# Kernel tuning notes

Hardware: AMD Instinct MI355X
Metric: run time of the kernel (lower is better)

## Reference

```python
import jax, jax.numpy as jnp
import numpy as np

N = 400000   # nodes; must equal E because the original code computes `out + x` with out per-edge
E = 400000   # edges
HID = 128
HEADS = 4
NEG_SLOPE = 0.01  # torch F.leaky_relu default


def setup_inputs() -> dict:
    key = jax.random.key(0)
    k1, k2, k3, k4 = jax.random.split(key, 4)
    x = jax.random.normal(k1, (N, HID), dtype=jnp.float32)
    edge_index = jax.random.randint(k2, (2, E), 0, N, dtype=jnp.int64)
    # xavier-uniform-ish scale for the attention parameter [1, heads, 2*hidden]
    lim_a = float(np.sqrt(6.0 / (1 + HEADS * 2 * HID)))
    attention = jax.random.uniform(k3, (1, HEADS, 2 * HID), jnp.float32, -lim_a, lim_a)
    lim_w = float(np.sqrt(1.0 / (HID * HEADS)))
    W = jax.random.uniform(k4, (HID, HID * HEADS), jnp.float32, -lim_w, lim_w)
    b = jnp.zeros((HID,), jnp.float32)
    return {"x": x, "edge_index": edge_index, "attention": attention, "W": W, "b": b}


def _scatter_softmax(s, seg, num_segments):
    # softmax over edges grouped by destination node index `seg` (axis 0)
    m = jax.lax.stop_gradient(jax.ops.segment_max(s, seg, num_segments=num_segments))
    ex = jnp.exp(s - m[seg])
    denom = jax.ops.segment_sum(ex, seg, num_segments=num_segments)
    return ex / denom[seg]


def reference(x, edge_index, attention, W, b):
    row, col = edge_index[0], edge_index[1]
    # [E, 2*HID] per-edge concatenated features
    ef = jnp.concatenate([x[row], x[col]], axis=-1)
    # per-head scores: (ef[:,None,:] * attention).sum(-1) -> [E, HEADS]
    scores = jnp.einsum('ef,hf->eh', ef, attention[0])
    scores = jax.nn.leaky_relu(scores, NEG_SLOPE)
    scores = jax.nn.softmax(scores, axis=1)      # softmax across heads (as in source)
    # dropout(p=0.1) -> identity in eval mode
    alpha = _scatter_softmax(scores, row, N)     # [E, HEADS] per-destination softmax
    # per-head weighted source features, concatenated over heads -> [E, HEADS*HID]
    feats = (alpha[:, :, None] * x[col][:, None, :]).reshape(E, HEADS * HID)
    out = feats @ W.T + b                        # Linear(hidden*heads -> hidden)
    return out + x
```

## Files before the change

kernel.cpp:

```cpp
#include <hip/hip_runtime.h>

#define NN 400000
#define NE 400000

typedef __attribute__((ext_vector_type(4))) float f32x4;
typedef __attribute__((ext_vector_type(8))) short s16x8;
typedef unsigned short ushort_t;

__device__ __forceinline__ ushort_t f2bf(float f) {
    union { float f; unsigned int u; } c;
    c.f = f;
    unsigned int u = c.u;
    u = u + 0x7fffu + ((u >> 16) & 1u);
    return (ushort_t)(u >> 16);
}
__device__ __forceinline__ float bf2f(ushort_t v) {
    union { unsigned int u; float f; } c;
    c.u = ((unsigned int)v) << 16;
    return c.f;
}

__global__ void k_detect(const int* __restrict__ ei_raw, int* __restrict__ flag) {
    if (threadIdx.x == 0 && blockIdx.x == 0) {
        int is64 = 1;
        for (int i = 0; i < 64; i++)
            if (ei_raw[2 * i + 1] != 0) { is64 = 0; break; }
        flag[0] = is64;
    }
}

__global__ void k_cvt_idx(const int* __restrict__ ei_raw, const int* __restrict__ flag,
                          int* __restrict__ ei32) {
    const int i = blockIdx.x * 256 + threadIdx.x;
    const int f = flag[0];
    ei32[i] = f ? ei_raw[2 * i] : ei_raw[i];
}

__global__ void k_wcvt(const float* __restrict__ W, ushort_t* __restrict__ wsw) {
    const int t = blockIdx.x * 256 + threadIdx.x;
    const int c = t >> 13;
    const int h = c >> 1, half = c & 1;
    const int si = t & 8191;
    const int i = si >> 6;
    const int inner = (si * 2) & 127;
    const int koff = inner ^ ((i & 7) << 4);
    const int j = half * 64 + (koff >> 1);
    wsw[t] = f2bf(W[i * 512 + h * 128 + j]);
}

__global__ void k_uv_cvt(const float* __restrict__ x, const float* __restrict__ att,
                         ushort_t* __restrict__ xbf, float* __restrict__ uv) {
    const int lane = threadIdx.x & 63;
    const int wid = threadIdx.x >> 6;
    const int g = lane & 15;
    const int ns = lane >> 4;

    float areg[8][8];
#pragma unroll
    for (int h = 0; h < 4; h++) {
        const f32x4 fa = *(const f32x4*)(att + h * 256 + g * 8);
        const f32x4 fb = *(const f32x4*)(att + h * 256 + g * 8 + 4);
        const f32x4 ba = *(const f32x4*)(att + h * 256 + 128 + g * 8);
        const f32x4 bb = *(const f32x4*)(att + h * 256 + 128 + g * 8 + 4);
#pragma unroll
        for (int m = 0; m < 4; m++) {
            areg[h][m] = fa[m];     areg[h][4 + m] = fb[m];
            areg[4 + h][m] = ba[m]; areg[4 + h][4 + m] = bb[m];
        }
    }

    for (int tile = blockIdx.x; tile < NN / 32; tile += gridDim.x) {
        const int nb = tile * 32 + wid * 8 + ns;
#pragma unroll
        for (int t = 0; t < 2; t++) {
            const int n = nb + t * 4;
            const f32x4 xa = *(const f32x4*)(x + (size_t)n * 128 + g * 8);
            const f32x4 xb = *(const f32x4*)(x + (size_t)n * 128 + g * 8 + 4);
            s16x8 pk;
#pragma unroll
            for (int m = 0; m < 4; m++) { pk[m] = (short)f2bf(xa[m]); pk[4 + m] = (short)f2bf(xb[m]); }
            *(s16x8*)(xbf + (size_t)n * 128 + g * 8) = pk;
            float r[8];
#pragma unroll
            for (int v = 0; v < 8; v++) {
                float s = 0.f;
#pragma unroll
                for (int m = 0; m < 4; m++) s += xa[m] * areg[v][m];
#pragma unroll
                for (int m = 0; m < 4; m++) s += xb[m] * areg[v][4 + m];
                r[v] = s;
            }
#pragma unroll
            for (int mask = 1; mask <= 4; mask <<= 1)
#pragma unroll
                for (int v = 0; v < 8; v++) r[v] += __shfl_xor(r[v], mask, 64);
            const int gv = g & 7;
            float s = r[0];
#pragma unroll
            for (int v = 1; v < 8; v++) s = (gv == v) ? r[v] : s;
            s += __shfl_xor(s, 8, 64);
            if (g < 8) uv[(size_t)n * 8 + g] = s;
        }
    }
}

__global__ void k_edge(const int* __restrict__ ei, const float* __restrict__ uv,
                       float* __restrict__ p, float* __restrict__ denom) {
    const int e = blockIdx.x * 256 + threadIdx.x;
    if (e >= NE) return;
    const int row = ei[e];
    const int col = ei[NE + e];
    const f32x4 u = *(const f32x4*)(uv + (size_t)row * 8);
    const f32x4 v = *(const f32x4*)(uv + (size_t)col * 8 + 4);
    float s[4];
    float mx = -1e30f;
#pragma unroll
    for (int h = 0; h < 4; h++) {
        float t = u[h] + v[h];
        t = t > 0.f ? t : 0.01f * t;
        s[h] = t;
        mx = fmaxf(mx, t);
    }
    float ex[4], sum = 0.f;
#pragma unroll
    for (int h = 0; h < 4; h++) { ex[h] = __expf(s[h] - mx); sum += ex[h]; }
    const float inv = 1.f / sum;
    f32x4 pv;
#pragma unroll
    for (int h = 0; h < 4; h++) pv[h] = __expf(ex[h] * inv);
    *(f32x4*)(p + (size_t)e * 4) = pv;
#pragma unroll
    for (int h = 0; h < 4; h++) atomicAdd(denom + (size_t)row * 4 + h, pv[h]);
}

__global__ void k_alpha(const int* __restrict__ ei, const float* __restrict__ p,
                        const float* __restrict__ denom, float* __restrict__ alpha_t) {
    const int e = blockIdx.x * 256 + threadIdx.x;
    if (e >= NE) return;
    const int row = ei[e];
    const f32x4 pv = *(const f32x4*)(p + (size_t)e * 4);
    const f32x4 dv = *(const f32x4*)(denom + (size_t)row * 4);
#pragma unroll
    for (int h = 0; h < 4; h++) alpha_t[(size_t)h * NE + e] = pv[h] / dv[h];
}

__global__ __launch_bounds__(512) void k_gemm(
    const ushort_t* __restrict__ xbf, const int* __restrict__ ei,
    const float* __restrict__ alpha_t, const ushort_t* __restrict__ wsw,
    const float* __restrict__ bias, float* __restrict__ out)
{
    __shared__ __align__(16) ushort_t Asm[128 * 128];
    __shared__ __align__(16) ushort_t Bsm[2][128 * 64];

    const int tid = threadIdx.x;
    const int lane = tid & 63;
    const int wid = tid >> 6;
    const int wr = wid >> 1;
    const int wc = wid & 1;
    const int e0 = blockIdx.x * 128;

#define B_ISSUE(c, buf) do {                                                         \
    const ushort_t* base_ = wsw + (c) * 8192;                                        \
    _Pragma("unroll")                                                                \
    for (int sub_ = 0; sub_ < 2; sub_++) {                                           \
        const int woff_ = wid * 2048 + sub_ * 1024;                                  \
        __builtin_amdgcn_global_load_lds(                                            \
            (const __attribute__((address_space(1))) unsigned int*)(base_ + woff_ / 2 + lane * 8), \
            (__attribute__((address_space(3))) unsigned int*)((char*)Bsm[buf] + woff_), \
            16, 0, 0);                                                               \
    } } while (0)

    {
        const int e_loc = tid >> 2, part = tid & 3;
        const int col = ei[NE + e0 + e_loc];
        const ushort_t* src = xbf + (size_t)col * 128 + part * 32;
#pragma unroll
        for (int q = 0; q < 4; q++) {
            const s16x8 v = *(const s16x8*)(src + q * 8);
            const int byte = (e_loc * 256 + part * 64 + q * 16) ^ ((e_loc & 7) << 4);
            *(s16x8*)((char*)Asm + byte) = v;
        }
    }
    B_ISSUE(0, 0);
    __syncthreads();

    s16x8 afr[4][2];
#pragma unroll
    for (int jq = 0; jq < 4; jq++)
#pragma unroll
        for (int eb = 0; eb < 2; eb++) {
            const int row = wr * 32 + eb * 16 + (lane & 15);
            const int byte = (row * 256 + jq * 64 + (lane >> 4) * 16) ^ ((row & 7) << 4);
            afr[jq][eb] = *(const s16x8*)((const char*)Asm + byte);
        }

    f32x4 fin[2][4];
#pragma unroll
    for (int eb = 0; eb < 2; eb++)
#pragma unroll
        for (int ib = 0; ib < 4; ib++) fin[eb][ib] = {0.f, 0.f, 0.f, 0.f};

#pragma unroll
    for (int h = 0; h < 4; h++) {
        f32x4 acc[2][4];
#pragma unroll
        for (int half = 0; half < 2; half++) {
            const int c = h * 2 + half;
            if (c < 7) B_ISSUE(c + 1, (c + 1) & 1);
#pragma unroll
            for (int ks = 0; ks < 2; ks++) {
                const int jq = half * 2 + ks;
#pragma unroll
                for (int ib = 0; ib < 4; ib++) {
                    const int row = wc * 64 + ib * 16 + (lane & 15);
                    const int byte = (row * 128 + ks * 64 + (lane >> 4) * 16) ^ ((row & 7) << 4);
                    const s16x8 bfr = *(const s16x8*)((const char*)Bsm[c & 1] + byte);
#pragma unroll
                    for (int eb = 0; eb < 2; eb++) {
                        if (jq == 0)
                            acc[eb][ib] = __builtin_amdgcn_mfma_f32_16x16x32_bf16(
                                afr[0][eb], bfr, (f32x4){0.f, 0.f, 0.f, 0.f}, 0, 0, 0);
                        else
                            acc[eb][ib] = __builtin_amdgcn_mfma_f32_16x16x32_bf16(
                                afr[jq][eb], bfr, acc[eb][ib], 0, 0, 0);
                    }
                }
            }
            __syncthreads();
        }
#pragma unroll
        for (int eb = 0; eb < 2; eb++) {
            const int ebase = wr * 32 + eb * 16 + (lane >> 4) * 4;
            const f32x4 av = *(const f32x4*)(alpha_t + (size_t)h * NE + e0 + ebase);
#pragma unroll
            for (int ib = 0; ib < 4; ib++)
#pragma unroll
                for (int r = 0; r < 4; r++) fin[eb][ib][r] += av[r] * acc[eb][ib][r];
        }
    }

#pragma unroll
    for (int ib = 0; ib < 4; ib++) {
        const int i = wc * 64 + ib * 16 + (lane & 15);
        const float bb = bias[i];
#pragma unroll
        for (int eb = 0; eb < 2; eb++) {
#pragma unroll
            for (int r = 0; r < 4; r++) {
                const int e = e0 + wr * 32 + eb * 16 + (lane >> 4) * 4 + r;
                const size_t off = (size_t)e * 128 + i;
                out[off] = fin[eb][ib][r] + bb + bf2f(xbf[off]);
            }
        }
    }
#undef B_ISSUE
}

extern "C" void kernel_launch(void* const* d_in, const int* in_sizes, int n_in,
                              void* d_out, int out_size, void* d_ws, size_t ws_size,
                              hipStream_t stream) {
    const float* x      = (const float*)d_in[0];
    const int*   ei_raw = (const int*)d_in[1];
    const float* att    = (const float*)d_in[2];
    const float* W      = (const float*)d_in[3];
    const float* b      = (const float*)d_in[4];
    float* out = (float*)d_out;

    char* ws = (char*)d_ws;
    float*    uv      = (float*)(ws);
    float*    p       = (float*)(ws + 12800000);
    float*    denom   = (float*)(ws + 19200000);
    float*    alpha_t = (float*)(ws + 25600000);
    ushort_t* wsw     = (ushort_t*)(ws + 32000000);
    int*      flag    = (int*)(ws + 32200000);
    int*      ei32    = (int*)(ws + 32200064);
    ushort_t* xbf     = (ushort_t*)(ws + 35400192);

    hipMemsetAsync(denom, 0, (size_t)NN * 4 * sizeof(float), stream);
    k_detect<<<1, 64, 0, stream>>>(ei_raw, flag);
    k_cvt_idx<<<2 * NE / 256, 256, 0, stream>>>(ei_raw, flag, ei32);
    k_wcvt<<<256, 256, 0, stream>>>(W, wsw);
    k_uv_cvt<<<2048, 256, 0, stream>>>(x, att, xbf, uv);
    k_edge<<<(NE + 255) / 256, 256, 0, stream>>>(ei32, uv, p, denom);
    k_alpha<<<(NE + 255) / 256, 256, 0, stream>>>(ei32, p, denom, alpha_t);
    k_gemm<<<NE / 128, 512, 0, stream>>>(xbf, ei32, alpha_t, wsw, b, out);
}
```

Measured before the change: 310.4 us.

## Hold W in registers and stream gathered x tiles in a persistent GEMM loop

The GEMM kernel is restructured so each wave keeps its slice of the bf16 weight matrix resident in registers for all four heads. Each block then loops over 25 tiles of 32 edges, gathering x rows from global memory straight into MFMA fragments with double buffering. This removes the per-block LDS staging of A and B and the repeated global_load_lds of W with its barriers. The costs are higher register pressure (launch bounds of 512 threads with 2 blocks), uncoalesced 16-byte gathers per lane, and fewer blocks (500) to cover the GPU.

```diff
diff --git a/kernel.cpp b/kernel.cpp
--- a/kernel.cpp
+++ b/kernel.cpp
@@ -36,16 +36,9 @@
     ei32[i] = f ? ei_raw[2 * i] : ei_raw[i];
 }
 
-__global__ void k_wcvt(const float* __restrict__ W, ushort_t* __restrict__ wsw) {
-    const int t = blockIdx.x * 256 + threadIdx.x;
-    const int c = t >> 13;
-    const int h = c >> 1, half = c & 1;
-    const int si = t & 8191;
-    const int i = si >> 6;
-    const int inner = (si * 2) & 127;
-    const int koff = inner ^ ((i & 7) << 4);
-    const int j = half * 64 + (koff >> 1);
-    wsw[t] = f2bf(W[i * 512 + h * 128 + j]);
+__global__ void k_wcvt(const float* __restrict__ W, ushort_t* __restrict__ wbf) {
+    const int i = blockIdx.x * 256 + threadIdx.x;
+    wbf[i] = f2bf(W[i]);
 }
 
 __global__ void k_uv_cvt(const float* __restrict__ x, const float* __restrict__ att,
@@ -144,116 +137,92 @@
     for (int h = 0; h < 4; h++) alpha_t[(size_t)h * NE + e] = pv[h] / dv[h];
 }
 
-__global__ __launch_bounds__(512) void k_gemm(
+__global__ __launch_bounds__(512, 2) void k_gemm(
     const ushort_t* __restrict__ xbf, const int* __restrict__ ei,
-    const float* __restrict__ alpha_t, const ushort_t* __restrict__ wsw,
+    const float* __restrict__ alpha_t, const ushort_t* __restrict__ wbf,
     const float* __restrict__ bias, float* __restrict__ out)
 {
-    __shared__ __align__(16) ushort_t Asm[128 * 128];
-    __shared__ __align__(16) ushort_t Bsm[2][128 * 64];
+    __shared__ int col_s[800];
+    __shared__ float alp_s[4][800];
 
     const int tid = threadIdx.x;
     const int lane = tid & 63;
     const int wid = tid >> 6;
-    const int wr = wid >> 1;
-    const int wc = wid & 1;
-    const int e0 = blockIdx.x * 128;
-
-#define B_ISSUE(c, buf) do {                                                         \
-    const ushort_t* base_ = wsw + (c) * 8192;                                        \
-    _Pragma("unroll")                                                                \
-    for (int sub_ = 0; sub_ < 2; sub_++) {                                           \
-        const int woff_ = wid * 2048 + sub_ * 1024;                                  \
-        __builtin_amdgcn_global_load_lds(                                            \
-            (const __attribute__((address_space(1))) unsigned int*)(base_ + woff_ / 2 + lane * 8), \
-            (__attribute__((address_space(3))) unsigned int*)((char*)Bsm[buf] + woff_), \
-            16, 0, 0);                                                               \
-    } } while (0)
-
+    const int e0 = blockIdx.x * 800;
+
+    for (int j = tid; j < 800; j += 512) col_s[j] = ei[NE + e0 + j];
+#pragma unroll
+    for (int h = 0; h < 4; h++)
+        for (int j = tid; j < 800; j += 512) alp_s[h][j] = alpha_t[(size_t)h * NE + e0 + j];
+
+    s16x8 bfr[4][4];
     {
-        const int e_loc = tid >> 2, part = tid & 3;
-        const int col = ei[NE + e0 + e_loc];
-        const ushort_t* src = xbf + (size_t)col * 128 + part * 32;
-#pragma unroll
-        for (int q = 0; q < 4; q++) {
-            const s16x8 v = *(const s16x8*)(src + q * 8);
-            const int byte = (e_loc * 256 + part * 64 + q * 16) ^ ((e_loc & 7) << 4);
-            *(s16x8*)((char*)Asm + byte) = v;
-        }
-    }
-    B_ISSUE(0, 0);
+        const ushort_t* bbase = wbf + (wid * 16 + (lane & 15)) * 512 + (lane >> 4) * 8;
+#pragma unroll
+        for (int h = 0; h < 4; h++)
+#pragma unroll
+            for (int ks = 0; ks < 4; ks++)
+                bfr[h][ks] = *(const s16x8*)(bbase + h * 128 + ks * 32);
+    }
+    const float bias_r = bias[wid * 16 + (lane & 15)];
     __syncthreads();
 
-    s16x8 afr[4][2];
-#pragma unroll
-    for (int jq = 0; jq < 4; jq++)
+    const f32x4 zero = {0.f, 0.f, 0.f, 0.f};
+    s16x8 afA[2][4], afB[2][4];
+
+    auto LOADA = [&](int t, s16x8 (&af)[2][4]) {
 #pragma unroll
         for (int eb = 0; eb < 2; eb++) {
-            const int row = wr * 32 + eb * 16 + (lane & 15);
-            const int byte = (row * 256 + jq * 64 + (lane >> 4) * 16) ^ ((row & 7) << 4);
-            afr[jq][eb] = *(const s16x8*)((const char*)Asm + byte);
-        }
-
-    f32x4 fin[2][4];
-#pragma unroll
-    for (int eb = 0; eb < 2; eb++)
-#pragma unroll
-        for (int ib = 0; ib < 4; ib++) fin[eb][ib] = {0.f, 0.f, 0.f, 0.f};
-
-#pragma unroll
-    for (int h = 0; h < 4; h++) {
-        f32x4 acc[2][4];
-#pragma unroll
-        for (int half = 0; half < 2; half++) {
-            const int c = h * 2 + half;
-            if (c < 7) B_ISSUE(c + 1, (c + 1) & 1);
-#pragma unroll
-            for (int ks = 0; ks < 2; ks++) {
-                const int jq = half * 2 + ks;
-#pragma unroll
-                for (int ib = 0; ib < 4; ib++) {
-                    const int row = wc * 64 + ib * 16 + (lane & 15);
-                    const int byte = (row * 128 + ks * 64 + (lane >> 4) * 16) ^ ((row & 7) << 4);
-                    const s16x8 bfr = *(const s16x8*)((const char*)Bsm[c & 1] + byte);
-#pragma unroll
-                    for (int eb = 0; eb < 2; eb++) {
-                        if (jq == 0)
-                            acc[eb][ib] = __builtin_amdgcn_mfma_f32_16x16x32_bf16(
-                                afr[0][eb], bfr, (f32x4){0.f, 0.f, 0.f, 0.f}, 0, 0, 0);
-                        else
-                            acc[eb][ib] = __builtin_amdgcn_mfma_f32_16x16x32_bf16(
-                                afr[jq][eb], bfr, acc[eb][ib], 0, 0, 0);
-                    }
-                }
-            }
-            __syncthreads();
-        }
-#pragma unroll
-        for (int eb = 0; eb < 2; eb++) {
-            const int ebase = wr * 32 + eb * 16 + (lane >> 4) * 4;
-            const f32x4 av = *(const f32x4*)(alpha_t + (size_t)h * NE + e0 + ebase);
-#pragma unroll
-            for (int ib = 0; ib < 4; ib++)
-#pragma unroll
-                for (int r = 0; r < 4; r++) fin[eb][ib][r] += av[r] * acc[eb][ib][r];
-        }
-    }
-
-#pragma unroll
-    for (int ib = 0; ib < 4; ib++) {
-        const int i = wc * 64 + ib * 16 + (lane & 15);
-        const float bb = bias[i];
-#pragma unroll
-        for (int eb = 0; eb < 2; eb++) {
-#pragma unroll
-            for (int r = 0; r < 4; r++) {
-                const int e = e0 + wr * 32 + eb * 16 + (lane >> 4) * 4 + r;
+            const int c = col_s[t * 32 + eb * 16 + (lane & 15)];
+            const ushort_t* base = xbf + (size_t)c * 128 + (lane >> 4) * 8;
+#pragma unroll
+            for (int jq = 0; jq < 4; jq++)
+                af[eb][jq] = *(const s16x8*)(base + jq * 32);
+        }
+    };
+
+    auto TILE = [&](int t, s16x8 (&af)[2][4]) {
+        f32x4 fin0 = zero, fin1 = zero;
+#pragma unroll
+        for (int h = 0; h < 4; h++) {
+            f32x4 a0 = __builtin_amdgcn_mfma_f32_16x16x32_bf16(af[0][0], bfr[h][0], zero, 0, 0, 0);
+            f32x4 a1 = __builtin_amdgcn_mfma_f32_16x16x32_bf16(af[1][0], bfr[h][0], zero, 0, 0, 0);
+#pragma unroll
+            for (int ks = 1; ks < 4; ks++) {
+                a0 = __builtin_amdgcn_mfma_f32_16x16x32_bf16(af[0][ks], bfr[h][ks], a0, 0, 0, 0);
+                a1 = __builtin_amdgcn_mfma_f32_16x16x32_bf16(af[1][ks], bfr[h][ks], a1, 0, 0, 0);
+            }
+            const f32x4 av0 = *(const f32x4*)&alp_s[h][t * 32 + (lane >> 4) * 4];
+            const f32x4 av1 = *(const f32x4*)&alp_s[h][t * 32 + 16 + (lane >> 4) * 4];
+            fin0 += av0 * a0;
+            fin1 += av1 * a1;
+        }
+        const int i = wid * 16 + (lane & 15);
+#pragma unroll
+        for (int r = 0; r < 4; r++) {
+            {
+                const int e = e0 + t * 32 + (lane >> 4) * 4 + r;
                 const size_t off = (size_t)e * 128 + i;
-                out[off] = fin[eb][ib][r] + bb + bf2f(xbf[off]);
-            }
-        }
-    }
-#undef B_ISSUE
+                out[off] = fin0[r] + bias_r + bf2f(xbf[off]);
+            }
+            {
+                const int e = e0 + t * 32 + 16 + (lane >> 4) * 4 + r;
+                const size_t off = (size_t)e * 128 + i;
+                out[off] = fin1[r] + bias_r + bf2f(xbf[off]);
+            }
+        }
+    };
+
+    LOADA(0, afA);
+#pragma unroll 1
+    for (int t = 0; t < 25; t += 2) {
+        if (t + 1 < 25) LOADA(t + 1, afB);
+        TILE(t, afA);
+        if (t + 1 < 25) {
+            if (t + 2 < 25) LOADA(t + 2, afA);
+            TILE(t + 1, afB);
+        }
+    }
 }
 
 extern "C" void kernel_launch(void* const* d_in, const int* in_sizes, int n_in,
@@ -271,7 +240,7 @@
     float*    p       = (float*)(ws + 12800000);
     float*    denom   = (float*)(ws + 19200000);
     float*    alpha_t = (float*)(ws + 25600000);
-    ushort_t* wsw     = (ushort_t*)(ws + 32000000);
+    ushort_t* wbf     = (ushort_t*)(ws + 32000000);
     int*      flag    = (int*)(ws + 32200000);
     int*      ei32    = (int*)(ws + 32200064);
     ushort_t* xbf     = (ushort_t*)(ws + 35400192);
@@ -279,9 +248,9 @@
     hipMemsetAsync(denom, 0, (size_t)NN * 4 * sizeof(float), stream);
     k_detect<<<1, 64, 0, stream>>>(ei_raw, flag);
     k_cvt_idx<<<2 * NE / 256, 256, 0, stream>>>(ei_raw, flag, ei32);
-    k_wcvt<<<256, 256, 0, stream>>>(W, wsw);
+    k_wcvt<<<256, 256, 0, stream>>>(W, wbf);
     k_uv_cvt<<<2048, 256, 0, stream>>>(x, att, xbf, uv);
     k_edge<<<(NE + 255) / 256, 256, 0, stream>>>(ei32, uv, p, denom);
     k_alpha<<<(NE + 255) / 256, 256, 0, stream>>>(ei32, p, denom, alpha_t);
-    k_gemm<<<NE / 128, 512, 0, stream>>>(xbf, ei32, alpha_t, wsw, b, out);
-}
+    k_gemm<<<NE / 800, 512, 0, stream>>>(xbf, ei32, alpha_t, wbf, b, out);
+}
```

Result: slower. 436.6 us (+40.6%).
